# Optimization experiments

Measured on AMD Instinct MI355X. Metric: run time of the kernel, lower is better.

Reference implementation:

```python
import jax, jax.numpy as jnp
import numpy as np

N_NODES = 50000
N_EDGES = 800000
NFEAT, NHID, NCLASS = 512, 128, 40
PN_SCALE = 1.0


def spmm(edge_row, edge_col, edge_val, h):
    # sparse [N,N] @ dense [N,F]: out[r] += val * h[c] for each edge (r, c)
    msgs = edge_val[:, None] * h[edge_col]  # [E, F]
    return jax.ops.segment_sum(msgs, edge_row, num_segments=N_NODES)


def pair_norm(x):
    # mode 'PN': center columns, scale by mean row norm
    x = x - x.mean(axis=0)
    rownorm_mean = jnp.sqrt(1e-6 + (x * x).sum(axis=1).mean())
    return PN_SCALE * x / rownorm_mean


def setup_inputs() -> dict:
    key = jax.random.key(0)
    ks = jax.random.split(key, 12)

    def uinit(k, shape, fan_out):
        stdv = 1.0 / np.sqrt(fan_out)
        return jax.random.uniform(k, shape, jnp.float32, -stdv, stdv)

    return {
        "x": jax.random.normal(ks[0], (N_NODES, NFEAT), jnp.float32),
        "edge_row": jax.random.randint(ks[1], (N_EDGES,), 0, N_NODES),
        "edge_col": jax.random.randint(ks[2], (N_EDGES,), 0, N_NODES),
        "edge_val": jax.random.uniform(ks[3], (N_EDGES,), jnp.float32),
        "W0": uinit(ks[4], (NFEAT, NHID), NHID),
        "b0": uinit(ks[5], (1, NHID), NHID),
        "W1": uinit(ks[6], (NHID, NHID), NHID),
        "b1": uinit(ks[7], (1, NHID), NHID),
        "W2": uinit(ks[8], (NHID, NHID), NHID),
        "b2": uinit(ks[9], (1, NHID), NHID),
        "W_out": uinit(ks[10], (NHID, NCLASS), NCLASS),
        "b_out": uinit(ks[11], (1, NCLASS), NCLASS),
    }


def reference(x, edge_row, edge_col, edge_val,
              W0, b0, W1, b1, W2, b2, W_out, b_out):
    # DeepGCN forward, eval mode (dropout p=0 is identity), residual=1 -> skip every layer
    x_old = 0.0
    for W, b in ((W0, b0), (W1, b1), (W2, b2)):
        h = x @ W                             # dense mm
        h = spmm(edge_row, edge_col, edge_val, h) + b  # sparse aggregate + bias
        h = pair_norm(h)
        h = jax.nn.relu(h)
        h = h + x_old                         # residual (x_old=0 on first layer)
        x_old = h
        x = h
    out = spmm(edge_row, edge_col, edge_val, x @ W_out) + b_out
    return out
```

## Files before the change

kernel.cpp:

```cpp
#include <hip/hip_runtime.h>
#include <hip/hip_bf16.h>
#include <math.h>

#define N_NODES 50000
#define N_EDGES 800000
#define NFEAT   512
#define NHID    128
#define NCLASS  40
#define NPASS    4
#define ROWS_PER_PASS (N_NODES / NPASS)
#define NCB      8
#define CB_W     (N_NODES / NCB)
#define NCNT     (N_NODES * NCB)
#define SCAN_BLOCKS ((NCNT + 1023) / 1024)
#define NSTAT    132
#define SPMM_BLOCKS 1024

typedef short bf16x8 __attribute__((ext_vector_type(8)));
typedef float f32x4  __attribute__((ext_vector_type(4)));

__device__ inline float bf2f(unsigned short u) {
    union { unsigned int i; float f; } x; x.i = ((unsigned int)u) << 16; return x.f;
}

__global__ void hist_kernel(const int* __restrict__ rows, const int* __restrict__ cols,
                            int* __restrict__ cnt, int n) {
    int i = blockIdx.x * blockDim.x + threadIdx.x;
    if (i < n) {
        int r = rows[i];
        int cb = cols[i] / CB_W;
        atomicAdd(&cnt[r * NCB + cb], 1);
    }
}

__global__ __launch_bounds__(1024) void scan_p1_kernel(const int* __restrict__ cnt,
                                                       int* __restrict__ bsum, int n) {
    int i = blockIdx.x * 1024 + threadIdx.x;
    int v = (i < n) ? cnt[i] : 0;
    __shared__ int sm[16];
    int lane = threadIdx.x & 63, w = threadIdx.x >> 6;
    #pragma unroll
    for (int off = 32; off > 0; off >>= 1) v += __shfl_xor(v, off, 64);
    if (lane == 0) sm[w] = v;
    __syncthreads();
    if (threadIdx.x == 0) {
        int s = 0;
        #pragma unroll
        for (int j = 0; j < 16; ++j) s += sm[j];
        bsum[blockIdx.x] = s;
    }
}

__global__ __launch_bounds__(512) void scan_p2_kernel(int* __restrict__ bsum, int nb) {
    __shared__ int wsum[8];
    int t = threadIdx.x;
    int lane = t & 63, w = t >> 6;
    int v = (t < nb) ? bsum[t] : 0;
    int x = v;
    #pragma unroll
    for (int off = 1; off < 64; off <<= 1) {
        int y = __shfl_up(x, off, 64);
        if (lane >= off) x += y;
    }
    if (lane == 63) wsum[w] = x;
    __syncthreads();
    int wbase = 0;
    for (int j = 0; j < w; ++j) wbase += wsum[j];
    if (t < nb) bsum[t] = wbase + x - v;
}

__global__ __launch_bounds__(1024) void scan_p3_kernel(const int* __restrict__ cnt,
                                                       const int* __restrict__ bsum,
                                                       int* __restrict__ bptr,
                                                       int* __restrict__ cursor, int n) {
    __shared__ int wsum[16];
    int b = blockIdx.x;
    int i = b * 1024 + threadIdx.x;
    int lane = threadIdx.x & 63, w = threadIdx.x >> 6;
    int v = (i < n) ? cnt[i] : 0;
    int x = v;
    #pragma unroll
    for (int off = 1; off < 64; off <<= 1) {
        int y = __shfl_up(x, off, 64);
        if (lane >= off) x += y;
    }
    if (lane == 63) wsum[w] = x;
    __syncthreads();
    int wbase = 0;
    for (int j = 0; j < w; ++j) wbase += wsum[j];
    int incl = bsum[b] + wbase + x;
    if (i < n) {
        bptr[i + 1] = incl;
        cursor[i] = incl - v;
    }
    if (i == 0) bptr[0] = 0;
}

__global__ void scatter_kernel(const int* __restrict__ rows, const int* __restrict__ cols,
                               const float* __restrict__ vals, int* __restrict__ cursor,
                               int2* __restrict__ csr_cv, int n, int blocksPerPass) {
    int p = blockIdx.x / blocksPerPass;
    int b = blockIdx.x % blocksPerPass;
    int i = b * 256 + threadIdx.x;
    if (i >= n) return;
    int r = rows[i];
    int lo = p * ROWS_PER_PASS;
    if (r < lo || r >= lo + ROWS_PER_PASS) return;
    int c = cols[i];
    int pos = atomicAdd(&cursor[r * NCB + c / CB_W], 1);
    csr_cv[pos] = make_int2(c, __float_as_int(vals[i]));
}

__global__ __launch_bounds__(256) void wt_cvt_all_kernel(const float* __restrict__ W0,
        const float* __restrict__ W1, const float* __restrict__ W2,
        const float* __restrict__ Wo, __hip_bfloat16* __restrict__ Wt0,
        __hip_bfloat16* __restrict__ Wt1, __hip_bfloat16* __restrict__ Wt2,
        __hip_bfloat16* __restrict__ Wot) {
    int i = blockIdx.x * blockDim.x + threadIdx.x;
    if (i < 65536) {
        int k = i >> 7, n = i & 127;
        Wt0[(size_t)n * 512 + k] = __float2bfloat16(W0[i]);
    } else if (i < 65536 + 16384) {
        int j = i - 65536; int k = j >> 7, n = j & 127;
        Wt1[(size_t)n * 128 + k] = __float2bfloat16(W1[j]);
    } else if (i < 65536 + 32768) {
        int j = i - 65536 - 16384; int k = j >> 7, n = j & 127;
        Wt2[(size_t)n * 128 + k] = __float2bfloat16(W2[j]);
    } else if (i < 65536 + 32768 + 8192) {
        int j = i - 65536 - 32768; int k = j >> 6, n = j & 63;
        float v = (n < NCLASS) ? Wo[k * NCLASS + n] : 0.f;
        Wot[(size_t)n * 128 + k] = __float2bfloat16(v);
    }
}

template<int BM, int BN, int K>
__global__ __launch_bounds__(256) void mfma_gemm_f32a(const float* __restrict__ Xg,
                                                      const __hip_bfloat16* __restrict__ Wt,
                                                      __hip_bfloat16* __restrict__ Ob,
                                                      float* __restrict__ stats_out, int M) {
    constexpr int BK  = 64;
    constexpr int LDK = 72;
    constexpr int WN  = BN / 64;
    __shared__ short As[BM * LDK];
    __shared__ short Bs[BN * LDK];
    int t = threadIdx.x;
    if (blockIdx.x == 0 && t < NSTAT) stats_out[t] = 0.f;
    int lane = t & 63;
    int w = t >> 6;
    int wm = w / WN, wn = w % WN;
    int row0 = blockIdx.x * BM;
    int m0 = wm * 32, n0 = wn * 64;
    int l15 = lane & 15, quad = lane >> 4;

    f32x4 acc[2][4] = {};

    for (int k0 = 0; k0 < K; k0 += BK) {
        #pragma unroll
        for (int idx = t; idx < BM * 16; idx += 256) {
            int r = idx >> 4, c = idx & 15;
            float4 v = make_float4(0.f, 0.f, 0.f, 0.f);
            if (row0 + r < M)
                v = *(const float4*)(Xg + (size_t)(row0 + r) * K + k0 + c * 4);
            __hip_bfloat16 o[4] = {__float2bfloat16(v.x), __float2bfloat16(v.y),
                                   __float2bfloat16(v.z), __float2bfloat16(v.w)};
            *(short4*)(As + r * LDK + c * 4) = *(short4*)o;
        }
        #pragma unroll
        for (int idx = t; idx < BN * 8; idx += 256) {
            int r = idx >> 3, c = idx & 7;
            uint4 v = *(const uint4*)(Wt + (size_t)r * K + k0 + c * 8);
            *(uint4*)(Bs + r * LDK + c * 8) = v;
        }
        __syncthreads();
        #pragma unroll
        for (int ks = 0; ks < 2; ++ks) {
            bf16x8 af[2], bfv[4];
            #pragma unroll
            for (int mt = 0; mt < 2; ++mt)
                af[mt] = *(const bf16x8*)(As + (m0 + mt * 16 + l15) * LDK + ks * 32 + quad * 8);
            #pragma unroll
            for (int nt = 0; nt < 4; ++nt)
                bfv[nt] = *(const bf16x8*)(Bs + (n0 + nt * 16 + l15) * LDK + ks * 32 + quad * 8);
            #pragma unroll
            for (int mt = 0; mt < 2; ++mt)
                #pragma unroll
                for (int nt = 0; nt < 4; ++nt)
                    acc[mt][nt] = __builtin_amdgcn_mfma_f32_16x16x32_bf16(
                        af[mt], bfv[nt], acc[mt][nt], 0, 0, 0);
        }
        __syncthreads();
    }
    #pragma unroll
    for (int mt = 0; mt < 2; ++mt) {
        #pragma unroll
        for (int reg = 0; reg < 4; ++reg) {
            int row = row0 + m0 + mt * 16 + quad * 4 + reg;
            if (row < M) {
                #pragma unroll
                for (int nt = 0; nt < 4; ++nt)
                    Ob[(size_t)row * BN + n0 + nt * 16 + l15] =
                        __float2bfloat16(acc[mt][nt][reg]);
            }
        }
    }
}

template<int BM, int BN, bool ADD_RESID, bool WRITE_X>
__global__ __launch_bounds__(256) void mfma_gemm_pn(const __hip_bfloat16* __restrict__ Bm,
                                                    __hip_bfloat16* __restrict__ Xb,
                                                    const float* __restrict__ stats_in,
                                                    float* __restrict__ stats_out,
                                                    const __hip_bfloat16* __restrict__ Wt,
                                                    __hip_bfloat16* __restrict__ Ob, int M) {
    constexpr int K = 128, BK = 64, LDK = 72;
    constexpr int WN = BN / 64;
    __shared__ short As[BM * LDK];
    __shared__ short Bs[BN * LDK];
    __shared__ float smu[128];
    __shared__ float sred[128];
    __shared__ float sscale;
    int t = threadIdx.x;
    if (stats_out && blockIdx.x == 0 && t < NSTAT) stats_out[t] = 0.f;
    if (t < 128) {
        float mu = stats_in[t] * (1.0f / N_NODES);
        smu[t] = mu;
        sred[t] = mu * mu;
    }
    __syncthreads();
    for (int off = 64; off > 0; off >>= 1) {
        if (t < off) sred[t] += sred[t + off];
        __syncthreads();
    }
    if (t == 0) {
        float ms = stats_in[128] * (1.0f / N_NODES) - sred[0];
        sscale = 1.0f / sqrtf(1e-6f + ms);
    }
    __syncthreads();
    float sc = sscale;

    int lane = t & 63;
    int w = t >> 6;
    int wm = w / WN, wn = w % WN;
    int row0 = blockIdx.x * BM;
    int m0 = wm * 32, n0 = wn * 64;
    int l15 = lane & 15, quad = lane >> 4;

    f32x4 acc[2][4] = {};

    for (int k0 = 0; k0 < K; k0 += BK) {
        #pragma unroll
        for (int idx = t; idx < BM * 8; idx += 256) {
            int r = idx >> 3, c = idx & 7;
            int gr = row0 + r;
            int k = k0 + c * 8;
            uint4 bm = make_uint4(0u, 0u, 0u, 0u);
            uint4 xo = make_uint4(0u, 0u, 0u, 0u);
            bool ok = gr < M;
            if (ok) bm = *(const uint4*)(Bm + (size_t)gr * 128 + k);
            if (ADD_RESID && ok) xo = *(const uint4*)(Xb + (size_t)gr * 128 + k);
            unsigned short* bu = (unsigned short*)&bm;
            unsigned short* xu = (unsigned short*)&xo;
            __hip_bfloat16 o[8];
            #pragma unroll
            for (int j = 0; j < 8; ++j) {
                float v = fmaxf((bf2f(bu[j]) - smu[k + j]) * sc, 0.f);
                if (ADD_RESID) v += bf2f(xu[j]);
                o[j] = __float2bfloat16(v);
            }
            *(uint4*)(As + r * LDK + c * 8) = *(uint4*)o;
            if (WRITE_X && ok) *(uint4*)(Xb + (size_t)gr * 128 + k) = *(uint4*)o;
        }
        #pragma unroll
        for (int idx = t; idx < BN * 8; idx += 256) {
            int r = idx >> 3, c = idx & 7;
            uint4 v = *(const uint4*)(Wt + (size_t)r * K + k0 + c * 8);
            *(uint4*)(Bs + r * LDK + c * 8) = v;
        }
        __syncthreads();
        #pragma unroll
        for (int ks = 0; ks < 2; ++ks) {
            bf16x8 af[2], bfv[4];
            #pragma unroll
            for (int mt = 0; mt < 2; ++mt)
                af[mt] = *(const bf16x8*)(As + (m0 + mt * 16 + l15) * LDK + ks * 32 + quad * 8);
            #pragma unroll
            for (int nt = 0; nt < 4; ++nt)
                bfv[nt] = *(const bf16x8*)(Bs + (n0 + nt * 16 + l15) * LDK + ks * 32 + quad * 8);
            #pragma unroll
            for (int mt = 0; mt < 2; ++mt)
                #pragma unroll
                for (int nt = 0; nt < 4; ++nt)
                    acc[mt][nt] = __builtin_amdgcn_mfma_f32_16x16x32_bf16(
                        af[mt], bfv[nt], acc[mt][nt], 0, 0, 0);
        }
        __syncthreads();
    }
    #pragma unroll
    for (int mt = 0; mt < 2; ++mt) {
        #pragma unroll
        for (int reg = 0; reg < 4; ++reg) {
            int row = row0 + m0 + mt * 16 + quad * 4 + reg;
            if (row < M) {
                #pragma unroll
                for (int nt = 0; nt < 4; ++nt)
                    Ob[(size_t)row * BN + n0 + nt * 16 + l15] =
                        __float2bfloat16(acc[mt][nt][reg]);
            }
        }
    }
}

__global__ __launch_bounds__(256) void spmm_bf16_kernel(const __hip_bfloat16* __restrict__ H,
                                                        const int* __restrict__ bptr,
                                                        const int2* __restrict__ cv,
                                                        const float* __restrict__ bias,
                                                        __hip_bfloat16* __restrict__ Bm,
                                                        float* __restrict__ stats,
                                                        int nrows) {
    __shared__ float sm[129];
    int t = threadIdx.x;
    if (t < 129) sm[t] = 0.f;
    __syncthreads();
    int lane = t & 63;
    int h = lane >> 5;
    int sub = lane & 31;
    int wid0 = (int)((blockIdx.x * 256 + t) >> 6);
    wid0 = __builtin_amdgcn_readfirstlane(wid0);
    const int NW = SPMM_BLOCKS * 4;
    const ushort4* H4 = (const ushort4*)H;
    float4 b4 = *(const float4*)(bias + 4 * sub);
    f32x4 csum = {0.f, 0.f, 0.f, 0.f};
    float sq = 0.f;

    for (int wid = wid0; wid < nrows; wid += NW) {
        int s = bptr[wid * NCB];
        int e = bptr[wid * NCB + NCB];
        f32x4 acc = {0.f, 0.f, 0.f, 0.f};
        int i = s;
        for (; i + 7 < e; i += 8) {
            int2 c0 = cv[i],     c1 = cv[i + 1], c2 = cv[i + 2], c3 = cv[i + 3];
            int2 c4 = cv[i + 4], c5 = cv[i + 5], c6 = cv[i + 6], c7 = cv[i + 7];
            int   ka = h ? c4.x : c0.x;  float va = __int_as_float(h ? c4.y : c0.y);
            int   kb = h ? c5.x : c1.x;  float vb = __int_as_float(h ? c5.y : c1.y);
            int   kc = h ? c6.x : c2.x;  float vc = __int_as_float(h ? c6.y : c2.y);
            int   kd = h ? c7.x : c3.x;  float vd = __int_as_float(h ? c7.y : c3.y);
            ushort4 ga = H4[(size_t)ka * 32 + sub];
            ushort4 gb = H4[(size_t)kb * 32 + sub];
            ushort4 gc = H4[(size_t)kc * 32 + sub];
            ushort4 gd = H4[(size_t)kd * 32 + sub];
            acc[0] = fmaf(va, bf2f(ga.x), acc[0]); acc[1] = fmaf(va, bf2f(ga.y), acc[1]);
            acc[2] = fmaf(va, bf2f(ga.z), acc[2]); acc[3] = fmaf(va, bf2f(ga.w), acc[3]);
            acc[0] = fmaf(vb, bf2f(gb.x), acc[0]); acc[1] = fmaf(vb, bf2f(gb.y), acc[1]);
            acc[2] = fmaf(vb, bf2f(gb.z), acc[2]); acc[3] = fmaf(vb, bf2f(gb.w), acc[3]);
            acc[0] = fmaf(vc, bf2f(gc.x), acc[0]); acc[1] = fmaf(vc, bf2f(gc.y), acc[1]);
            acc[2] = fmaf(vc, bf2f(gc.z), acc[2]); acc[3] = fmaf(vc, bf2f(gc.w), acc[3]);
            acc[0] = fmaf(vd, bf2f(gd.x), acc[0]); acc[1] = fmaf(vd, bf2f(gd.y), acc[1]);
            acc[2] = fmaf(vd, bf2f(gd.z), acc[2]); acc[3] = fmaf(vd, bf2f(gd.w), acc[3]);
        }
        for (; i + 3 < e; i += 4) {
            int2 c0 = cv[i], c1 = cv[i + 1], c2 = cv[i + 2], c3 = cv[i + 3];
            int   ka = h ? c2.x : c0.x;  float va = __int_as_float(h ? c2.y : c0.y);
            int   kb = h ? c3.x : c1.x;  float vb = __int_as_float(h ? c3.y : c1.y);
            ushort4 ga = H4[(size_t)ka * 32 + sub];
            ushort4 gb = H4[(size_t)kb * 32 + sub];
            acc[0] = fmaf(va, bf2f(ga.x), acc[0]); acc[1] = fmaf(va, bf2f(ga.y), acc[1]);
            acc[2] = fmaf(va, bf2f(ga.z), acc[2]); acc[3] = fmaf(va, bf2f(ga.w), acc[3]);
            acc[0] = fmaf(vb, bf2f(gb.x), acc[0]); acc[1] = fmaf(vb, bf2f(gb.y), acc[1]);
            acc[2] = fmaf(vb, bf2f(gb.z), acc[2]); acc[3] = fmaf(vb, bf2f(gb.w), acc[3]);
        }
        for (; i < e; ++i) {
            int2 c = cv[i];
            if (h == 0) {
                float v = __int_as_float(c.y);
                ushort4 g = H4[(size_t)c.x * 32 + sub];
                acc[0] = fmaf(v, bf2f(g.x), acc[0]); acc[1] = fmaf(v, bf2f(g.y), acc[1]);
                acc[2] = fmaf(v, bf2f(g.z), acc[2]); acc[3] = fmaf(v, bf2f(g.w), acc[3]);
            }
        }
        #pragma unroll
        for (int c = 0; c < 4; ++c) acc[c] += __shfl_xor(acc[c], 32);
        if (h == 0) {
            float v0 = acc[0] + b4.x, v1 = acc[1] + b4.y;
            float v2 = acc[2] + b4.z, v3 = acc[3] + b4.w;
            __hip_bfloat16 o[4] = {__float2bfloat16(v0), __float2bfloat16(v1),
                                   __float2bfloat16(v2), __float2bfloat16(v3)};
            *(ushort4*)(Bm + (size_t)wid * 128 + 4 * sub) = *(ushort4*)o;
            csum[0] += v0; csum[1] += v1; csum[2] += v2; csum[3] += v3;
            sq = fmaf(v0, v0, sq); sq = fmaf(v1, v1, sq);
            sq = fmaf(v2, v2, sq); sq = fmaf(v3, v3, sq);
        }
    }
    if (h == 0) {
        #pragma unroll
        for (int j = 0; j < 4; ++j) atomicAdd(&sm[4 * sub + j], csum[j]);
        atomicAdd(&sm[128], sq);
    }
    __syncthreads();
    if (t < 129) atomicAdd(&stats[t], sm[t]);
}

__global__ __launch_bounds__(256) void spmm_out_kernel(const __hip_bfloat16* __restrict__ G,
                                                       const int* __restrict__ bptr,
                                                       const int2* __restrict__ cv,
                                                       const float* __restrict__ bias,
                                                       float* __restrict__ out, int nrows) {
    int wid = (int)((blockIdx.x * blockDim.x + threadIdx.x) >> 6);
    wid = __builtin_amdgcn_readfirstlane(wid);
    int lane = threadIdx.x & 63;
    int h = lane >> 5;
    int sub = lane & 31;
    if (wid >= nrows) return;
    int s = bptr[wid * NCB];
    int e = bptr[wid * NCB + NCB];
    const __hip_bfloat162* G2 = (const __hip_bfloat162*)G;
    float a0 = 0.f, a1 = 0.f;
    int i = s;
    for (; i + 7 < e; i += 8) {
        int2 c0 = cv[i],     c1 = cv[i + 1], c2 = cv[i + 2], c3 = cv[i + 3];
        int2 c4 = cv[i + 4], c5 = cv[i + 5], c6 = cv[i + 6], c7 = cv[i + 7];
        int   ka = h ? c4.x : c0.x;  float va = __int_as_float(h ? c4.y : c0.y);
        int   kb = h ? c5.x : c1.x;  float vb = __int_as_float(h ? c5.y : c1.y);
        int   kc = h ? c6.x : c2.x;  float vc = __int_as_float(h ? c6.y : c2.y);
        int   kd = h ? c7.x : c3.x;  float vd = __int_as_float(h ? c7.y : c3.y);
        __hip_bfloat162 ga = G2[(size_t)ka * 32 + sub];
        __hip_bfloat162 gb = G2[(size_t)kb * 32 + sub];
        __hip_bfloat162 gc = G2[(size_t)kc * 32 + sub];
        __hip_bfloat162 gd = G2[(size_t)kd * 32 + sub];
        a0 = fmaf(va, __bfloat162float(ga.x), a0); a1 = fmaf(va, __bfloat162float(ga.y), a1);
        a0 = fmaf(vb, __bfloat162float(gb.x), a0); a1 = fmaf(vb, __bfloat162float(gb.y), a1);
        a0 = fmaf(vc, __bfloat162float(gc.x), a0); a1 = fmaf(vc, __bfloat162float(gc.y), a1);
        a0 = fmaf(vd, __bfloat162float(gd.x), a0); a1 = fmaf(vd, __bfloat162float(gd.y), a1);
    }
    for (; i + 3 < e; i += 4) {
        int2 c0 = cv[i], c1 = cv[i + 1], c2 = cv[i + 2], c3 = cv[i + 3];
        int   ka = h ? c2.x : c0.x;  float va = __int_as_float(h ? c2.y : c0.y);
        int   kb = h ? c3.x : c1.x;  float vb = __int_as_float(h ? c3.y : c1.y);
        __hip_bfloat162 ga = G2[(size_t)ka * 32 + sub];
        __hip_bfloat162 gb = G2[(size_t)kb * 32 + sub];
        a0 = fmaf(va, __bfloat162float(ga.x), a0); a1 = fmaf(va, __bfloat162float(ga.y), a1);
        a0 = fmaf(vb, __bfloat162float(gb.x), a0); a1 = fmaf(vb, __bfloat162float(gb.y), a1);
    }
    for (; i < e; ++i) {
        int2 c = cv[i];
        if (h == 0) {
            float v = __int_as_float(c.y);
            __hip_bfloat162 g = G2[(size_t)c.x * 32 + sub];
            a0 = fmaf(v, __bfloat162float(g.x), a0);
            a1 = fmaf(v, __bfloat162float(g.y), a1);
        }
    }
    a0 += __shfl_xor(a0, 32);
    a1 += __shfl_xor(a1, 32);
    if (h == 0 && sub < NCLASS / 2) {
        float2 b2 = *(const float2*)(bias + 2 * sub);
        float2 o = make_float2(a0 + b2.x, a1 + b2.y);
        *(float2*)(out + (size_t)wid * NCLASS + 2 * sub) = o;
    }
}

extern "C" void kernel_launch(void* const* d_in, const int* in_sizes, int n_in,
                              void* d_out, int out_size, void* d_ws, size_t ws_size,
                              hipStream_t stream) {
    const float* x        = (const float*)d_in[0];
    const int*   edge_row = (const int*)  d_in[1];
    const int*   edge_col = (const int*)  d_in[2];
    const float* edge_val = (const float*)d_in[3];
    const float* W0 = (const float*)d_in[4];
    const float* b0 = (const float*)d_in[5];
    const float* W1 = (const float*)d_in[6];
    const float* b1 = (const float*)d_in[7];
    const float* W2 = (const float*)d_in[8];
    const float* b2 = (const float*)d_in[9];
    const float* W_out = (const float*)d_in[10];
    const float* b_out = (const float*)d_in[11];
    float* out = (float*)d_out;

    const size_t NH = (size_t)N_NODES * NHID;

    char* p = (char*)d_ws;
    __hip_bfloat16* Xb   = (__hip_bfloat16*)p;  p += NH * 2;
    __hip_bfloat16* A_bf = (__hip_bfloat16*)p;  p += NH * 2;
    __hip_bfloat16* Bm   = (__hip_bfloat16*)p;  p += NH * 2;
    __hip_bfloat16* Wt0 = (__hip_bfloat16*)p;   p += (size_t)128 * 512 * 2;
    __hip_bfloat16* Wt1 = (__hip_bfloat16*)p;   p += (size_t)128 * 128 * 2;
    __hip_bfloat16* Wt2 = (__hip_bfloat16*)p;   p += (size_t)128 * 128 * 2;
    __hip_bfloat16* Wot = (__hip_bfloat16*)p;   p += (size_t)64 * 128 * 2;
    float* statsA   = (float*)p;                p += NSTAT * 4;
    float* statsB   = (float*)p;                p += NSTAT * 4;
    int* cnt      = (int*)p;                    p += (size_t)NCNT * 4;
    int* bptr     = (int*)p;                    p += (size_t)(NCNT + 1) * 4 + 4;
    int* cursor   = (int*)p;                    p += (size_t)NCNT * 4;
    int* bsum     = (int*)p;                    p += (size_t)SCAN_BLOCKS * 4 + 4;
    int2* csr_cv  = (int2*)p;                   p += (size_t)N_EDGES * 8;

    const int EB = (N_EDGES + 255) / 256;

    wt_cvt_all_kernel<<<(65536 + 32768 + 8192 + 255) / 256, 256, 0, stream>>>(
        W0, W1, W2, W_out, Wt0, Wt1, Wt2, Wot);

    hipMemsetAsync(cnt, 0, NCNT * sizeof(int), stream);
    hist_kernel<<<EB, 256, 0, stream>>>(edge_row, edge_col, cnt, N_EDGES);
    scan_p1_kernel<<<SCAN_BLOCKS, 1024, 0, stream>>>(cnt, bsum, NCNT);
    scan_p2_kernel<<<1, 512, 0, stream>>>(bsum, SCAN_BLOCKS);
    scan_p3_kernel<<<SCAN_BLOCKS, 1024, 0, stream>>>(cnt, bsum, bptr, cursor, NCNT);
    scatter_kernel<<<EB * NPASS, 256, 0, stream>>>(edge_row, edge_col, edge_val, cursor,
                                                   csr_cv, N_EDGES, EB);

    mfma_gemm_f32a<64, 128, 512><<<(N_NODES + 63) / 64, 256, 0, stream>>>(
        x, Wt0, A_bf, statsA, N_NODES);
    spmm_bf16_kernel<<<SPMM_BLOCKS, 256, 0, stream>>>(A_bf, bptr, csr_cv, b0, Bm,
                                                      statsA, N_NODES);

    mfma_gemm_pn<64, 128, false, true><<<(N_NODES + 63) / 64, 256, 0, stream>>>(
        Bm, Xb, statsA, statsB, Wt1, A_bf, N_NODES);
    spmm_bf16_kernel<<<SPMM_BLOCKS, 256, 0, stream>>>(A_bf, bptr, csr_cv, b1, Bm,
                                                      statsB, N_NODES);

    mfma_gemm_pn<64, 128, true, true><<<(N_NODES + 63) / 64, 256, 0, stream>>>(
        Bm, Xb, statsB, statsA, Wt2, A_bf, N_NODES);
    spmm_bf16_kernel<<<SPMM_BLOCKS, 256, 0, stream>>>(A_bf, bptr, csr_cv, b2, Bm,
                                                      statsA, N_NODES);

    mfma_gemm_pn<128, 64, true, false><<<(N_NODES + 127) / 128, 256, 0, stream>>>(
        Bm, Xb, statsA, nullptr, Wot, A_bf, N_NODES);
    spmm_out_kernel<<<(N_NODES + 3) / 4, 256, 0, stream>>>(A_bf, bptr, csr_cv, b_out,
                                                           out, N_NODES);
}
```

Before: 509.4 us.

## Split PairNorm statistics out of SpMM into a separate reduction kernel

The SpMM kernel no longer runs as a persistent grid accumulating column sums and squared norms. It now launches one wavefront per row and only writes the bf16 aggregated output. A new stats_kernel re-reads the bf16 result to compute column sums and the sum of squares, with atomics into the stats buffer. This removes the per-block shared atomics and the persistent-loop structure, but adds an extra kernel launch and an extra pass over the activations per layer. Stats are now computed from bf16-rounded values rather than fp32, which slightly changes numerics.

```diff
diff --git a/kernel.cpp b/kernel.cpp
--- a/kernel.cpp
+++ b/kernel.cpp
@@ -14,7 +14,7 @@
 #define NCNT     (N_NODES * NCB)
 #define SCAN_BLOCKS ((NCNT + 1023) / 1024)
 #define NSTAT    132
-#define SPMM_BLOCKS 1024
+#define NB_STATS 256
 
 typedef short bf16x8 __attribute__((ext_vector_type(8)));
 typedef float f32x4  __attribute__((ext_vector_type(4)));
@@ -315,88 +315,96 @@
                                                         const int2* __restrict__ cv,
                                                         const float* __restrict__ bias,
                                                         __hip_bfloat16* __restrict__ Bm,
-                                                        float* __restrict__ stats,
                                                         int nrows) {
-    __shared__ float sm[129];
-    int t = threadIdx.x;
-    if (t < 129) sm[t] = 0.f;
-    __syncthreads();
-    int lane = t & 63;
+    int wid = (int)((blockIdx.x * blockDim.x + threadIdx.x) >> 6);
+    wid = __builtin_amdgcn_readfirstlane(wid);
+    int lane = threadIdx.x & 63;
     int h = lane >> 5;
     int sub = lane & 31;
-    int wid0 = (int)((blockIdx.x * 256 + t) >> 6);
-    wid0 = __builtin_amdgcn_readfirstlane(wid0);
-    const int NW = SPMM_BLOCKS * 4;
+    if (wid >= nrows) return;
+    int s = bptr[wid * NCB];
+    int e = bptr[wid * NCB + NCB];
     const ushort4* H4 = (const ushort4*)H;
-    float4 b4 = *(const float4*)(bias + 4 * sub);
-    f32x4 csum = {0.f, 0.f, 0.f, 0.f};
-    float sq = 0.f;
-
-    for (int wid = wid0; wid < nrows; wid += NW) {
-        int s = bptr[wid * NCB];
-        int e = bptr[wid * NCB + NCB];
-        f32x4 acc = {0.f, 0.f, 0.f, 0.f};
-        int i = s;
-        for (; i + 7 < e; i += 8) {
-            int2 c0 = cv[i],     c1 = cv[i + 1], c2 = cv[i + 2], c3 = cv[i + 3];
-            int2 c4 = cv[i + 4], c5 = cv[i + 5], c6 = cv[i + 6], c7 = cv[i + 7];
-            int   ka = h ? c4.x : c0.x;  float va = __int_as_float(h ? c4.y : c0.y);
-            int   kb = h ? c5.x : c1.x;  float vb = __int_as_float(h ? c5.y : c1.y);
-            int   kc = h ? c6.x : c2.x;  float vc = __int_as_float(h ? c6.y : c2.y);
-            int   kd = h ? c7.x : c3.x;  float vd = __int_as_float(h ? c7.y : c3.y);
-            ushort4 ga = H4[(size_t)ka * 32 + sub];
-            ushort4 gb = H4[(size_t)kb * 32 + sub];
-            ushort4 gc = H4[(size_t)kc * 32 + sub];
-            ushort4 gd = H4[(size_t)kd * 32 + sub];
-            acc[0] = fmaf(va, bf2f(ga.x), acc[0]); acc[1] = fmaf(va, bf2f(ga.y), acc[1]);
-            acc[2] = fmaf(va, bf2f(ga.z), acc[2]); acc[3] = fmaf(va, bf2f(ga.w), acc[3]);
-            acc[0] = fmaf(vb, bf2f(gb.x), acc[0]); acc[1] = fmaf(vb, bf2f(gb.y), acc[1]);
-            acc[2] = fmaf(vb, bf2f(gb.z), acc[2]); acc[3] = fmaf(vb, bf2f(gb.w), acc[3]);
-            acc[0] = fmaf(vc, bf2f(gc.x), acc[0]); acc[1] = fmaf(vc, bf2f(gc.y), acc[1]);
-            acc[2] = fmaf(vc, bf2f(gc.z), acc[2]); acc[3] = fmaf(vc, bf2f(gc.w), acc[3]);
-            acc[0] = fmaf(vd, bf2f(gd.x), acc[0]); acc[1] = fmaf(vd, bf2f(gd.y), acc[1]);
-            acc[2] = fmaf(vd, bf2f(gd.z), acc[2]); acc[3] = fmaf(vd, bf2f(gd.w), acc[3]);
-        }
-        for (; i + 3 < e; i += 4) {
-            int2 c0 = cv[i], c1 = cv[i + 1], c2 = cv[i + 2], c3 = cv[i + 3];
-            int   ka = h ? c2.x : c0.x;  float va = __int_as_float(h ? c2.y : c0.y);
-            int   kb = h ? c3.x : c1.x;  float vb = __int_as_float(h ? c3.y : c1.y);
-            ushort4 ga = H4[(size_t)ka * 32 + sub];
-            ushort4 gb = H4[(size_t)kb * 32 + sub];
-            acc[0] = fmaf(va, bf2f(ga.x), acc[0]); acc[1] = fmaf(va, bf2f(ga.y), acc[1]);
-            acc[2] = fmaf(va, bf2f(ga.z), acc[2]); acc[3] = fmaf(va, bf2f(ga.w), acc[3]);
-            acc[0] = fmaf(vb, bf2f(gb.x), acc[0]); acc[1] = fmaf(vb, bf2f(gb.y), acc[1]);
-            acc[2] = fmaf(vb, bf2f(gb.z), acc[2]); acc[3] = fmaf(vb, bf2f(gb.w), acc[3]);
-        }
-        for (; i < e; ++i) {
-            int2 c = cv[i];
-            if (h == 0) {
-                float v = __int_as_float(c.y);
-                ushort4 g = H4[(size_t)c.x * 32 + sub];
-                acc[0] = fmaf(v, bf2f(g.x), acc[0]); acc[1] = fmaf(v, bf2f(g.y), acc[1]);
-                acc[2] = fmaf(v, bf2f(g.z), acc[2]); acc[3] = fmaf(v, bf2f(g.w), acc[3]);
-            }
-        }
-        #pragma unroll
-        for (int c = 0; c < 4; ++c) acc[c] += __shfl_xor(acc[c], 32);
+    f32x4 acc = {0.f, 0.f, 0.f, 0.f};
+    int i = s;
+    for (; i + 7 < e; i += 8) {
+        int2 c0 = cv[i],     c1 = cv[i + 1], c2 = cv[i + 2], c3 = cv[i + 3];
+        int2 c4 = cv[i + 4], c5 = cv[i + 5], c6 = cv[i + 6], c7 = cv[i + 7];
+        int   ka = h ? c4.x : c0.x;  float va = __int_as_float(h ? c4.y : c0.y);
+        int   kb = h ? c5.x : c1.x;  float vb = __int_as_float(h ? c5.y : c1.y);
+        int   kc = h ? c6.x : c2.x;  float vc = __int_as_float(h ? c6.y : c2.y);
+        int   kd = h ? c7.x : c3.x;  float vd = __int_as_float(h ? c7.y : c3.y);
+        ushort4 ga = H4[(size_t)ka * 32 + sub];
+        ushort4 gb = H4[(size_t)kb * 32 + sub];
+        ushort4 gc = H4[(size_t)kc * 32 + sub];
+        ushort4 gd = H4[(size_t)kd * 32 + sub];
+        acc[0] = fmaf(va, bf2f(ga.x), acc[0]); acc[1] = fmaf(va, bf2f(ga.y), acc[1]);
+        acc[2] = fmaf(va, bf2f(ga.z), acc[2]); acc[3] = fmaf(va, bf2f(ga.w), acc[3]);
+        acc[0] = fmaf(vb, bf2f(gb.x), acc[0]); acc[1] = fmaf(vb, bf2f(gb.y), acc[1]);
+        acc[2] = fmaf(vb, bf2f(gb.z), acc[2]); acc[3] = fmaf(vb, bf2f(gb.w), acc[3]);
+        acc[0] = fmaf(vc, bf2f(gc.x), acc[0]); acc[1] = fmaf(vc, bf2f(gc.y), acc[1]);
+        acc[2] = fmaf(vc, bf2f(gc.z), acc[2]); acc[3] = fmaf(vc, bf2f(gc.w), acc[3]);
+        acc[0] = fmaf(vd, bf2f(gd.x), acc[0]); acc[1] = fmaf(vd, bf2f(gd.y), acc[1]);
+        acc[2] = fmaf(vd, bf2f(gd.z), acc[2]); acc[3] = fmaf(vd, bf2f(gd.w), acc[3]);
+    }
+    for (; i + 3 < e; i += 4) {
+        int2 c0 = cv[i], c1 = cv[i + 1], c2 = cv[i + 2], c3 = cv[i + 3];
+        int   ka = h ? c2.x : c0.x;  float va = __int_as_float(h ? c2.y : c0.y);
+        int   kb = h ? c3.x : c1.x;  float vb = __int_as_float(h ? c3.y : c1.y);
+        ushort4 ga = H4[(size_t)ka * 32 + sub];
+        ushort4 gb = H4[(size_t)kb * 32 + sub];
+        acc[0] = fmaf(va, bf2f(ga.x), acc[0]); acc[1] = fmaf(va, bf2f(ga.y), acc[1]);
+        acc[2] = fmaf(va, bf2f(ga.z), acc[2]); acc[3] = fmaf(va, bf2f(ga.w), acc[3]);
+        acc[0] = fmaf(vb, bf2f(gb.x), acc[0]); acc[1] = fmaf(vb, bf2f(gb.y), acc[1]);
+        acc[2] = fmaf(vb, bf2f(gb.z), acc[2]); acc[3] = fmaf(vb, bf2f(gb.w), acc[3]);
+    }
+    for (; i < e; ++i) {
+        int2 c = cv[i];
         if (h == 0) {
-            float v0 = acc[0] + b4.x, v1 = acc[1] + b4.y;
-            float v2 = acc[2] + b4.z, v3 = acc[3] + b4.w;
-            __hip_bfloat16 o[4] = {__float2bfloat16(v0), __float2bfloat16(v1),
-                                   __float2bfloat16(v2), __float2bfloat16(v3)};
-            *(ushort4*)(Bm + (size_t)wid * 128 + 4 * sub) = *(ushort4*)o;
-            csum[0] += v0; csum[1] += v1; csum[2] += v2; csum[3] += v3;
-            sq = fmaf(v0, v0, sq); sq = fmaf(v1, v1, sq);
-            sq = fmaf(v2, v2, sq); sq = fmaf(v3, v3, sq);
-        }
-    }
+            float v = __int_as_float(c.y);
+            ushort4 g = H4[(size_t)c.x * 32 + sub];
+            acc[0] = fmaf(v, bf2f(g.x), acc[0]); acc[1] = fmaf(v, bf2f(g.y), acc[1]);
+            acc[2] = fmaf(v, bf2f(g.z), acc[2]); acc[3] = fmaf(v, bf2f(g.w), acc[3]);
+        }
+    }
+    #pragma unroll
+    for (int c = 0; c < 4; ++c) acc[c] += __shfl_xor(acc[c], 32);
     if (h == 0) {
-        #pragma unroll
-        for (int j = 0; j < 4; ++j) atomicAdd(&sm[4 * sub + j], csum[j]);
-        atomicAdd(&sm[128], sq);
-    }
-    __syncthreads();
-    if (t < 129) atomicAdd(&stats[t], sm[t]);
+        float4 b4 = *(const float4*)(bias + 4 * sub);
+        __hip_bfloat16 o[4] = {__float2bfloat16(acc[0] + b4.x), __float2bfloat16(acc[1] + b4.y),
+                               __float2bfloat16(acc[2] + b4.z), __float2bfloat16(acc[3] + b4.w)};
+        *(ushort4*)(Bm + (size_t)wid * 128 + 4 * sub) = *(ushort4*)o;
+    }
+}
+
+__global__ __launch_bounds__(256) void stats_kernel(const __hip_bfloat16* __restrict__ B,
+                                                    float* __restrict__ stats, int n2) {
+    int tid = blockIdx.x * blockDim.x + threadIdx.x;
+    int stride = NB_STATS * 256;
+    const __hip_bfloat162* B2 = (const __hip_bfloat162*)B;
+    float cs0 = 0.f, cs1 = 0.f, sq = 0.f;
+    for (int j = tid; j < n2; j += stride) {
+        __hip_bfloat162 h = B2[j];
+        float a = __bfloat162float(h.x), b = __bfloat162float(h.y);
+        cs0 += a; cs1 += b;
+        sq = fmaf(a, a, sq); sq = fmaf(b, b, sq);
+    }
+    __shared__ float s0[256], s1[256], ss[256];
+    int t = threadIdx.x;
+    s0[t] = cs0; s1[t] = cs1; ss[t] = sq;
+    __syncthreads();
+    if (t < 64) {
+        float a = s0[t] + s0[t + 64] + s0[t + 128] + s0[t + 192];
+        float b = s1[t] + s1[t + 64] + s1[t + 128] + s1[t + 192];
+        atomicAdd(&stats[2 * t], a);
+        atomicAdd(&stats[2 * t + 1], b);
+    }
+    __syncthreads();
+    for (int off = 128; off > 0; off >>= 1) {
+        if (t < off) ss[t] += ss[t + off];
+        __syncthreads();
+    }
+    if (t == 0) atomicAdd(&stats[128], ss[0]);
 }
 
 __global__ __launch_bounds__(256) void spmm_out_kernel(const __hip_bfloat16* __restrict__ G,
@@ -494,6 +502,7 @@
     int2* csr_cv  = (int2*)p;                   p += (size_t)N_EDGES * 8;
 
     const int EB = (N_EDGES + 255) / 256;
+    const int SPMM_GRID = (N_NODES + 3) / 4;
 
     wt_cvt_all_kernel<<<(65536 + 32768 + 8192 + 255) / 256, 256, 0, stream>>>(
         W0, W1, W2, W_out, Wt0, Wt1, Wt2, Wot);
@@ -508,18 +517,18 @@
 
     mfma_gemm_f32a<64, 128, 512><<<(N_NODES + 63) / 64, 256, 0, stream>>>(
         x, Wt0, A_bf, statsA, N_NODES);
-    spmm_bf16_kernel<<<SPMM_BLOCKS, 256, 0, stream>>>(A_bf, bptr, csr_cv, b0, Bm,
-                                                      statsA, N_NODES);
+    spmm_bf16_kernel<<<SPMM_GRID, 256, 0, stream>>>(A_bf, bptr, csr_cv, b0, Bm, N_NODES);
+    stats_kernel<<<NB_STATS, 256, 0, stream>>>(Bm, statsA, (int)(NH / 2));
 
     mfma_gemm_pn<64, 128, false, true><<<(N_NODES + 63) / 64, 256, 0, stream>>>(
         Bm, Xb, statsA, statsB, Wt1, A_bf, N_NODES);
-    spmm_bf16_kernel<<<SPMM_BLOCKS, 256, 0, stream>>>(A_bf, bptr, csr_cv, b1, Bm,
-                                                      statsB, N_NODES);
+    spmm_bf16_kernel<<<SPMM_GRID, 256, 0, stream>>>(A_bf, bptr, csr_cv, b1, Bm, N_NODES);
+    stats_kernel<<<NB_STATS, 256, 0, stream>>>(Bm, statsB, (int)(NH / 2));
 
     mfma_gemm_pn<64, 128, true, true><<<(N_NODES + 63) / 64, 256, 0, stream>>>(
         Bm, Xb, statsB, statsA, Wt2, A_bf, N_NODES);
-    spmm_bf16_kernel<<<SPMM_BLOCKS, 256, 0, stream>>>(A_bf, bptr, csr_cv, b2, Bm,
-                                                      statsA, N_NODES);
+    spmm_bf16_kernel<<<SPMM_GRID, 256, 0, stream>>>(A_bf, bptr, csr_cv, b2, Bm, N_NODES);
+    stats_kernel<<<NB_STATS, 256, 0, stream>>>(Bm, statsA, (int)(NH / 2));
 
     mfma_gemm_pn<128, 64, true, false><<<(N_NODES + 127) / 128, 256, 0, stream>>>(
         Bm, Xb, statsA, nullptr, Wot, A_bf, N_NODES);
```

Measured after the change: 495.9 us. 1.03x faster.

## Fuse preprocessing kernels and slice PairNorm stats atomics across replicas

Applied to the files above, without the earlier changes.

The weight conversion is merged with the histogram kernel, and the edge scatter is merged into the first GEMM launch as extra blocks, which removes two launches and lets independent work overlap. The SpMM kernel goes from a persistent grid of 1024 blocks to one wavefront per row. Its column-sum and square-sum statistics are now spread over 16 slices that the next GEMM adds back together, so fewer blocks contend on the same global atomics. In exchange there are far more blocks, each issuing shared and global atomics, and every consumer has to read 16 slices.

```diff
diff --git a/kernel.cpp b/kernel.cpp
--- a/kernel.cpp
+++ b/kernel.cpp
@@ -13,8 +13,9 @@
 #define CB_W     (N_NODES / NCB)
 #define NCNT     (N_NODES * NCB)
 #define SCAN_BLOCKS ((NCNT + 1023) / 1024)
-#define NSTAT    132
-#define SPMM_BLOCKS 1024
+#define NSLICE   16
+#define SLICE_W  132
+#define WT_BLOCKS 416
 
 typedef short bf16x8 __attribute__((ext_vector_type(8)));
 typedef float f32x4  __attribute__((ext_vector_type(4)));
@@ -23,13 +24,36 @@
     union { unsigned int i; float f; } x; x.i = ((unsigned int)u) << 16; return x.f;
 }
 
-__global__ void hist_kernel(const int* __restrict__ rows, const int* __restrict__ cols,
-                            int* __restrict__ cnt, int n) {
-    int i = blockIdx.x * blockDim.x + threadIdx.x;
-    if (i < n) {
-        int r = rows[i];
-        int cb = cols[i] / CB_W;
-        atomicAdd(&cnt[r * NCB + cb], 1);
+__global__ __launch_bounds__(256) void wt_hist_kernel(const float* __restrict__ W0,
+        const float* __restrict__ W1, const float* __restrict__ W2,
+        const float* __restrict__ Wo, __hip_bfloat16* __restrict__ Wt0,
+        __hip_bfloat16* __restrict__ Wt1, __hip_bfloat16* __restrict__ Wt2,
+        __hip_bfloat16* __restrict__ Wot,
+        const int* __restrict__ rows, const int* __restrict__ cols,
+        int* __restrict__ cnt, int n) {
+    if (blockIdx.x >= WT_BLOCKS) {
+        int i = (blockIdx.x - WT_BLOCKS) * 256 + threadIdx.x;
+        if (i < n) {
+            int r = rows[i];
+            int cb = cols[i] / CB_W;
+            atomicAdd(&cnt[r * NCB + cb], 1);
+        }
+        return;
+    }
+    int i = blockIdx.x * 256 + threadIdx.x;
+    if (i < 65536) {
+        int k = i >> 7, n2 = i & 127;
+        Wt0[(size_t)n2 * 512 + k] = __float2bfloat16(W0[i]);
+    } else if (i < 65536 + 16384) {
+        int j = i - 65536; int k = j >> 7, n2 = j & 127;
+        Wt1[(size_t)n2 * 128 + k] = __float2bfloat16(W1[j]);
+    } else if (i < 65536 + 32768) {
+        int j = i - 65536 - 16384; int k = j >> 7, n2 = j & 127;
+        Wt2[(size_t)n2 * 128 + k] = __float2bfloat16(W2[j]);
+    } else if (i < 65536 + 32768 + 8192) {
+        int j = i - 65536 - 32768; int k = j >> 6, n2 = j & 63;
+        float v = (n2 < NCLASS) ? Wo[k * NCLASS + n2] : 0.f;
+        Wot[(size_t)n2 * 128 + k] = __float2bfloat16(v);
     }
 }
 
@@ -96,55 +120,37 @@
     if (i == 0) bptr[0] = 0;
 }
 
-__global__ void scatter_kernel(const int* __restrict__ rows, const int* __restrict__ cols,
-                               const float* __restrict__ vals, int* __restrict__ cursor,
-                               int2* __restrict__ csr_cv, int n, int blocksPerPass) {
-    int p = blockIdx.x / blocksPerPass;
-    int b = blockIdx.x % blocksPerPass;
-    int i = b * 256 + threadIdx.x;
-    if (i >= n) return;
-    int r = rows[i];
-    int lo = p * ROWS_PER_PASS;
-    if (r < lo || r >= lo + ROWS_PER_PASS) return;
-    int c = cols[i];
-    int pos = atomicAdd(&cursor[r * NCB + c / CB_W], 1);
-    csr_cv[pos] = make_int2(c, __float_as_int(vals[i]));
-}
-
-__global__ __launch_bounds__(256) void wt_cvt_all_kernel(const float* __restrict__ W0,
-        const float* __restrict__ W1, const float* __restrict__ W2,
-        const float* __restrict__ Wo, __hip_bfloat16* __restrict__ Wt0,
-        __hip_bfloat16* __restrict__ Wt1, __hip_bfloat16* __restrict__ Wt2,
-        __hip_bfloat16* __restrict__ Wot) {
-    int i = blockIdx.x * blockDim.x + threadIdx.x;
-    if (i < 65536) {
-        int k = i >> 7, n = i & 127;
-        Wt0[(size_t)n * 512 + k] = __float2bfloat16(W0[i]);
-    } else if (i < 65536 + 16384) {
-        int j = i - 65536; int k = j >> 7, n = j & 127;
-        Wt1[(size_t)n * 128 + k] = __float2bfloat16(W1[j]);
-    } else if (i < 65536 + 32768) {
-        int j = i - 65536 - 16384; int k = j >> 7, n = j & 127;
-        Wt2[(size_t)n * 128 + k] = __float2bfloat16(W2[j]);
-    } else if (i < 65536 + 32768 + 8192) {
-        int j = i - 65536 - 32768; int k = j >> 6, n = j & 63;
-        float v = (n < NCLASS) ? Wo[k * NCLASS + n] : 0.f;
-        Wot[(size_t)n * 128 + k] = __float2bfloat16(v);
-    }
-}
-
 template<int BM, int BN, int K>
-__global__ __launch_bounds__(256) void mfma_gemm_f32a(const float* __restrict__ Xg,
-                                                      const __hip_bfloat16* __restrict__ Wt,
-                                                      __hip_bfloat16* __restrict__ Ob,
-                                                      float* __restrict__ stats_out, int M) {
+__global__ __launch_bounds__(256) void gemm0_scatter_kernel(
+        const float* __restrict__ Xg, const __hip_bfloat16* __restrict__ Wt,
+        __hip_bfloat16* __restrict__ Ob, float* __restrict__ stats_out, int M,
+        const int* __restrict__ rows, const int* __restrict__ cols,
+        const float* __restrict__ vals, int* __restrict__ cursor,
+        int2* __restrict__ csr_cv, int n, int blocksPerPass, int gemmBlocks) {
     constexpr int BK  = 64;
     constexpr int LDK = 72;
     constexpr int WN  = BN / 64;
     __shared__ short As[BM * LDK];
     __shared__ short Bs[BN * LDK];
     int t = threadIdx.x;
-    if (blockIdx.x == 0 && t < NSTAT) stats_out[t] = 0.f;
+
+    if ((int)blockIdx.x >= gemmBlocks) {
+        int bb = blockIdx.x - gemmBlocks;
+        int p = bb / blocksPerPass;
+        int b = bb % blocksPerPass;
+        int i = b * 256 + t;
+        if (i >= n) return;
+        int r = rows[i];
+        int lo = p * ROWS_PER_PASS;
+        if (r < lo || r >= lo + ROWS_PER_PASS) return;
+        int c = cols[i];
+        int pos = atomicAdd(&cursor[r * NCB + c / CB_W], 1);
+        csr_cv[pos] = make_int2(c, __float_as_int(vals[i]));
+        return;
+    }
+
+    if (blockIdx.x == 0)
+        for (int z = t; z < NSLICE * SLICE_W; z += 256) stats_out[z] = 0.f;
     int lane = t & 63;
     int w = t >> 6;
     int wm = w / WN, wn = w % WN;
@@ -218,11 +224,17 @@
     __shared__ short Bs[BN * LDK];
     __shared__ float smu[128];
     __shared__ float sred[128];
+    __shared__ float ssq16[NSLICE];
     __shared__ float sscale;
     int t = threadIdx.x;
-    if (stats_out && blockIdx.x == 0 && t < NSTAT) stats_out[t] = 0.f;
+    if (stats_out && blockIdx.x == 0)
+        for (int z = t; z < NSLICE * SLICE_W; z += 256) stats_out[z] = 0.f;
+    if (t < NSLICE) ssq16[t] = stats_in[t * SLICE_W + 128];
     if (t < 128) {
-        float mu = stats_in[t] * (1.0f / N_NODES);
+        float cs = 0.f;
+        #pragma unroll
+        for (int s = 0; s < NSLICE; ++s) cs += stats_in[s * SLICE_W + t];
+        float mu = cs * (1.0f / N_NODES);
         smu[t] = mu;
         sred[t] = mu * mu;
     }
@@ -232,7 +244,10 @@
         __syncthreads();
     }
     if (t == 0) {
-        float ms = stats_in[128] * (1.0f / N_NODES) - sred[0];
+        float sq = 0.f;
+        #pragma unroll
+        for (int s = 0; s < NSLICE; ++s) sq += ssq16[s];
+        float ms = sq * (1.0f / N_NODES) - sred[0];
         sscale = 1.0f / sqrtf(1e-6f + ms);
     }
     __syncthreads();
@@ -321,20 +336,15 @@
     int t = threadIdx.x;
     if (t < 129) sm[t] = 0.f;
     __syncthreads();
+    int wid = (int)((blockIdx.x * blockDim.x + t) >> 6);
+    wid = __builtin_amdgcn_readfirstlane(wid);
     int lane = t & 63;
     int h = lane >> 5;
     int sub = lane & 31;
-    int wid0 = (int)((blockIdx.x * 256 + t) >> 6);
-    wid0 = __builtin_amdgcn_readfirstlane(wid0);
-    const int NW = SPMM_BLOCKS * 4;
-    const ushort4* H4 = (const ushort4*)H;
-    float4 b4 = *(const float4*)(bias + 4 * sub);
-    f32x4 csum = {0.f, 0.f, 0.f, 0.f};
-    float sq = 0.f;
-
-    for (int wid = wid0; wid < nrows; wid += NW) {
+    if (wid < nrows) {
         int s = bptr[wid * NCB];
         int e = bptr[wid * NCB + NCB];
+        const ushort4* H4 = (const ushort4*)H;
         f32x4 acc = {0.f, 0.f, 0.f, 0.f};
         int i = s;
         for (; i + 7 < e; i += 8) {
@@ -380,23 +390,25 @@
         #pragma unroll
         for (int c = 0; c < 4; ++c) acc[c] += __shfl_xor(acc[c], 32);
         if (h == 0) {
+            float4 b4 = *(const float4*)(bias + 4 * sub);
             float v0 = acc[0] + b4.x, v1 = acc[1] + b4.y;
             float v2 = acc[2] + b4.z, v3 = acc[3] + b4.w;
             __hip_bfloat16 o[4] = {__float2bfloat16(v0), __float2bfloat16(v1),
                                    __float2bfloat16(v2), __float2bfloat16(v3)};
             *(ushort4*)(Bm + (size_t)wid * 128 + 4 * sub) = *(ushort4*)o;
-            csum[0] += v0; csum[1] += v1; csum[2] += v2; csum[3] += v3;
-            sq = fmaf(v0, v0, sq); sq = fmaf(v1, v1, sq);
-            sq = fmaf(v2, v2, sq); sq = fmaf(v3, v3, sq);
-        }
-    }
-    if (h == 0) {
-        #pragma unroll
-        for (int j = 0; j < 4; ++j) atomicAdd(&sm[4 * sub + j], csum[j]);
-        atomicAdd(&sm[128], sq);
-    }
-    __syncthreads();
-    if (t < 129) atomicAdd(&stats[t], sm[t]);
+            atomicAdd(&sm[4 * sub + 0], v0);
+            atomicAdd(&sm[4 * sub + 1], v1);
+            atomicAdd(&sm[4 * sub + 2], v2);
+            atomicAdd(&sm[4 * sub + 3], v3);
+            float sq = v0 * v0 + v1 * v1 + v2 * v2 + v3 * v3;
+            #pragma unroll
+            for (int off = 16; off > 0; off >>= 1) sq += __shfl_down(sq, off, 32);
+            if (sub == 0) atomicAdd(&sm[128], sq);
+        }
+    }
+    __syncthreads();
+    if (t < 129)
+        atomicAdd(&stats[(blockIdx.x & (NSLICE - 1)) * SLICE_W + t], sm[t]);
 }
 
 __global__ __launch_bounds__(256) void spmm_out_kernel(const __hip_bfloat16* __restrict__ G,
@@ -485,8 +497,8 @@
     __hip_bfloat16* Wt1 = (__hip_bfloat16*)p;   p += (size_t)128 * 128 * 2;
     __hip_bfloat16* Wt2 = (__hip_bfloat16*)p;   p += (size_t)128 * 128 * 2;
     __hip_bfloat16* Wot = (__hip_bfloat16*)p;   p += (size_t)64 * 128 * 2;
-    float* statsA   = (float*)p;                p += NSTAT * 4;
-    float* statsB   = (float*)p;                p += NSTAT * 4;
+    float* statsA   = (float*)p;                p += (size_t)NSLICE * SLICE_W * 4;
+    float* statsB   = (float*)p;                p += (size_t)NSLICE * SLICE_W * 4;
     int* cnt      = (int*)p;                    p += (size_t)NCNT * 4;
     int* bptr     = (int*)p;                    p += (size_t)(NCNT + 1) * 4 + 4;
     int* cursor   = (int*)p;                    p += (size_t)NCNT * 4;
@@ -494,32 +506,31 @@
     int2* csr_cv  = (int2*)p;                   p += (size_t)N_EDGES * 8;
 
     const int EB = (N_EDGES + 255) / 256;
-
-    wt_cvt_all_kernel<<<(65536 + 32768 + 8192 + 255) / 256, 256, 0, stream>>>(
-        W0, W1, W2, W_out, Wt0, Wt1, Wt2, Wot);
+    const int SPMM_GRID = (N_NODES + 3) / 4;
+    const int GEMM0_BLOCKS = (N_NODES + 63) / 64;
 
     hipMemsetAsync(cnt, 0, NCNT * sizeof(int), stream);
-    hist_kernel<<<EB, 256, 0, stream>>>(edge_row, edge_col, cnt, N_EDGES);
+    wt_hist_kernel<<<WT_BLOCKS + EB, 256, 0, stream>>>(
+        W0, W1, W2, W_out, Wt0, Wt1, Wt2, Wot, edge_row, edge_col, cnt, N_EDGES);
     scan_p1_kernel<<<SCAN_BLOCKS, 1024, 0, stream>>>(cnt, bsum, NCNT);
     scan_p2_kernel<<<1, 512, 0, stream>>>(bsum, SCAN_BLOCKS);
     scan_p3_kernel<<<SCAN_BLOCKS, 1024, 0, stream>>>(cnt, bsum, bptr, cursor, NCNT);
-    scatter_kernel<<<EB * NPASS, 256, 0, stream>>>(edge_row, edge_col, edge_val, cursor,
-                                                   csr_cv, N_EDGES, EB);
-
-    mfma_gemm_f32a<64, 128, 512><<<(N_NODES + 63) / 64, 256, 0, stream>>>(
-        x, Wt0, A_bf, statsA, N_NODES);
-    spmm_bf16_kernel<<<SPMM_BLOCKS, 256, 0, stream>>>(A_bf, bptr, csr_cv, b0, Bm,
-                                                      statsA, N_NODES);
-
-    mfma_gemm_pn<64, 128, false, true><<<(N_NODES + 63) / 64, 256, 0, stream>>>(
+
+    gemm0_scatter_kernel<64, 128, 512><<<GEMM0_BLOCKS + EB * NPASS, 256, 0, stream>>>(
+        x, Wt0, A_bf, statsA, N_NODES,
+        edge_row, edge_col, edge_val, cursor, csr_cv, N_EDGES, EB, GEMM0_BLOCKS);
+    spmm_bf16_kernel<<<SPMM_GRID, 256, 0, stream>>>(A_bf, bptr, csr_cv, b0, Bm,
+                                                    statsA, N_NODES);
+
+    mfma_gemm_pn<64, 128, false, true><<<GEMM0_BLOCKS, 256, 0, stream>>>(
         Bm, Xb, statsA, statsB, Wt1, A_bf, N_NODES);
-    spmm_bf16_kernel<<<SPMM_BLOCKS, 256, 0, stream>>>(A_bf, bptr, csr_cv, b1, Bm,
-                                                      statsB, N_NODES);
-
-    mfma_gemm_pn<64, 128, true, true><<<(N_NODES + 63) / 64, 256, 0, stream>>>(
+    spmm_bf16_kernel<<<SPMM_GRID, 256, 0, stream>>>(A_bf, bptr, csr_cv, b1, Bm,
+                                                    statsB, N_NODES);
+
+    mfma_gemm_pn<64, 128, true, true><<<GEMM0_BLOCKS, 256, 0, stream>>>(
         Bm, Xb, statsB, statsA, Wt2, A_bf, N_NODES);
-    spmm_bf16_kernel<<<SPMM_BLOCKS, 256, 0, stream>>>(A_bf, bptr, csr_cv, b2, Bm,
-                                                      statsA, N_NODES);
+    spmm_bf16_kernel<<<SPMM_GRID, 256, 0, stream>>>(A_bf, bptr, csr_cv, b2, Bm,
+                                                    statsA, N_NODES);
 
     mfma_gemm_pn<128, 64, true, false><<<(N_NODES + 127) / 128, 256, 0, stream>>>(
         Bm, Xb, statsA, nullptr, Wot, A_bf, N_NODES);
```

Result: faster. 495.2 us (-2.8%).
